# Kernel tuning notes

Measured on AMD Instinct MI355X. Metric: run time of the kernel, lower is better.

Reference implementation:

```python
import jax, jax.numpy as jnp
import numpy as np

KS = 3  # kernel_size


def _im2col(x):
    # x: (N, C, H, W) -> (N, H*W, C*KS*KS), matching torch unfold (channel-major,
    # kernel-position-minor) ordering with padding=1.
    N, C, H, W = x.shape
    xp = jnp.pad(x, ((0, 0), (0, 0), (1, 1), (1, 1)))
    patches = jnp.stack(
        [xp[:, :, i:i + H, j:j + W] for i in range(KS) for j in range(KS)],
        axis=2,
    )  # (N, C, 9, H, W)
    return patches.reshape(N, C * KS * KS, H * W).transpose(0, 2, 1)


def setup_inputs() -> dict:
    key = jax.random.key(0)
    k1, k2, k3, k4, k5 = jax.random.split(key, 5)
    N, C, H, W = 4, 64, 192, 192
    outC = 3
    return {
        "lr_features": jax.random.normal(k1, (N, C, H, W), dtype=jnp.float32),
        "W1": jax.random.normal(k2, (3, 256), dtype=jnp.float32) * 0.05,
        "b1": jax.random.normal(k3, (256,), dtype=jnp.float32) * 0.05,
        "W2": jax.random.normal(k4, (256, KS * KS * C * outC), dtype=jnp.float32) * 0.05,
        "b2": jax.random.normal(k5, (KS * KS * C * outC,), dtype=jnp.float32) * 0.05,
        "sr_scale": 4,
    }


def reference(lr_features, W1, b1, W2, b2, sr_scale):
    # Integer sr_scale: mask_mat is all-true and pos_mat_small is the s*s grid
    # of sub-pixel offsets [1/s, i/s, j/s] for i, j in [0, s).
    N, C, H, W = lr_features.shape
    s = int(np.ceil(sr_scale))
    inv = 1.0 / float(sr_scale)
    off = jnp.arange(s, dtype=jnp.float32) * inv
    pos = jnp.stack(jnp.meshgrid(off, off, indexing="ij"), axis=-1).reshape(s * s, 2)
    pos = jnp.concatenate(
        [jnp.full((s * s, 1), inv, dtype=jnp.float32), pos], axis=1
    )  # (s^2, 3)

    # Pos2Weight MLP -> per-subpixel dynamic conv weights (s^2, C*9, outC)
    hidden = jax.nn.relu(pos @ W1 + b1)
    local_weight = (hidden @ W2 + b2).reshape(s * s, KS * KS * C, -1)
    outC = local_weight.shape[-1]

    cols = _im2col(lr_features)  # (N, H*W, C*9)
    # batched small matmul: each sub-pixel position has its own filter
    out = jnp.einsum("npk,sko->nspo", cols, local_weight)  # (N, s^2, H*W, outC)
    out = out.reshape(N, s, s, H, W, outC)
    out = out.transpose(0, 5, 3, 1, 4, 2).reshape(N, outC, s * H, s * W)
    return out
```

## Files before the change

### kernel.cpp

```cpp
#include <hip/hip_runtime.h>


#define HH   192
#define WWD  192
#define SS   4
#define OC   3
#define PO   48
#define HID  256
#define W2LD 1728

typedef short  bf16x8 __attribute__((ext_vector_type(8)));
typedef float  f32x4  __attribute__((ext_vector_type(4)));

static __device__ __forceinline__ short f2bf(float f) {
    unsigned u = __float_as_uint(f);
    unsigned r = (u + 0x7fffu + ((u >> 16) & 1u)) >> 16;
    return (short)r;
}

static __device__ __forceinline__ void pin(bf16x8& v) {
    asm volatile("" : "+v"(v));
}

__global__ __launch_bounds__(256) void prep_kernel(
        const float* __restrict__ x,
        const float* __restrict__ W1, const float* __restrict__ b1,
        const float* __restrict__ W2, const float* __restrict__ b2,
        short* __restrict__ lwb, short* __restrict__ xt) {
    const int b = blockIdx.x;
    const int t = threadIdx.x;
    if (b < 112) {
        __shared__ float hlds[HID];
        const int p = b / 7;
        {
            const float pi = (float)(p >> 2) * 0.25f;
            const float pj = (float)(p & 3) * 0.25f;
            const float v = 0.25f * W1[t] + pi * W1[HID + t] + pj * W1[2 * HID + t]
                          + b1[t];
            hlds[t] = v > 0.f ? v : 0.f;
        }
        __syncthreads();
        const int col = (b % 7) * 256 + t;
        if (col < W2LD) {
            float a = 0.f;
#pragma unroll 32
            for (int hh = 0; hh < HID; ++hh)
                a += hlds[hh] * W2[hh * W2LD + col];
            const int o = col % 3, kc = col / 3;
            const int tap = kc % 9, c = kc / 9;
            lwb[(tap * PO + p * 3 + o) * 64 + c] = f2bf(a + b2[col]);
        }
    } else {
        __shared__ short tl[64][72];
        const int bb = b - 112;
        const int wt = bb % 3;
        const int h  = (bb / 3) % HH;
        const int n  = bb / (3 * HH);
        const int w0 = wt * 64;
#pragma unroll
        for (int i = 0; i < 4; ++i) {
            const int idx = i * 256 + t;
            const int c   = idx >> 4;
            const int j4  = idx & 15;
            const float4 v = *(const float4*)
                &x[(((size_t)(n * 64 + c)) * HH + h) * WWD + w0 + j4 * 4];
            tl[j4 * 4 + 0][c] = f2bf(v.x);
            tl[j4 * 4 + 1][c] = f2bf(v.y);
            tl[j4 * 4 + 2][c] = f2bf(v.z);
            tl[j4 * 4 + 3][c] = f2bf(v.w);
        }
        __syncthreads();
        const int w  = t >> 2;
        const int c0 = (t & 3) * 16;
        short* dst = &xt[(((size_t)n * HH + h) * WWD + w0 + w) * 64 + c0];
        *(bf16x8*)&dst[0] = *(const bf16x8*)&tl[w][c0];
        *(bf16x8*)&dst[8] = *(const bf16x8*)&tl[w][c0 + 8];
    }
}

__global__ __launch_bounds__(192, 3) void meta_up_mfma(
        const short* __restrict__ xt, const short* __restrict__ lwb,
        float* __restrict__ out) {
    __shared__ __align__(16) short smem[3 * 66 * 64];
    short* xlds = smem;
    float* obuf = (float*)smem;

    const int strip = (blockIdx.x & 7) * 288 + (blockIdx.x >> 3);
    const int n   = strip / (HH * 3);
    const int rem = strip % (HH * 3);
    const int h   = rem / 3;
    const int wch = rem % 3;
    const int w0  = wch * 64;

    const int tid  = threadIdx.x;
    const int lane = tid & 63, wv = tid >> 6;
    const int quad = lane >> 4, l15 = lane & 15;

    bf16x8 Bfrag[18];
#pragma unroll
    for (int tap = 0; tap < 9; ++tap)
#pragma unroll
        for (int kc2 = 0; kc2 < 2; ++kc2)
            Bfrag[tap * 2 + kc2] = *(const bf16x8*)
                &lwb[(tap * PO + wv * 16 + l15) * 64 + kc2 * 32 + quad * 8];
#pragma unroll
    for (int i = 0; i < 18; ++i) pin(Bfrag[i]);

    {
        const int gr  = h + wv - 1;
        const bool rok = (unsigned)gr < (unsigned)HH;
        const short* __restrict__ src_row =
            xt + (size_t)(n * HH + (rok ? gr : 0)) * (WWD * 64);
        const bf16x8 z = {0, 0, 0, 0, 0, 0, 0, 0};
        bf16x8 vv[8];
#pragma unroll
        for (int i = 0; i < 8; ++i) {
            const int q  = i * 64 + lane;
            const int j  = q >> 3, cb = q & 7;
            const int gc = w0 - 1 + j;
            const bool ok = rok && ((unsigned)gc < (unsigned)WWD);
            vv[i] = ok ? *(const bf16x8*)&src_row[(size_t)(ok ? gc : 0) * 64 + cb * 8]
                       : z;
        }
#pragma unroll
        for (int i = 0; i < 8; ++i) {
            const int q = i * 64 + lane;
            const int j = q >> 3, cb = q & 7;
            *(bf16x8*)&xlds[(wv * 66 + j) * 64 + ((cb ^ (j & 7)) << 3)] = vv[i];
        }
        if (lane < 16) {
            const int q  = 512 + lane;
            const int j  = q >> 3, cb = q & 7;
            const int gc = w0 - 1 + j;
            const bool ok = rok && ((unsigned)gc < (unsigned)WWD);
            const bf16x8 v = ok ?
                *(const bf16x8*)&src_row[(size_t)(ok ? gc : 0) * 64 + cb * 8] : z;
            *(bf16x8*)&xlds[(wv * 66 + j) * 64 + ((cb ^ (j & 7)) << 3)] = v;
        }
    }
    __syncthreads();

    f32x4 acc[4];
#pragma unroll
    for (int mt = 0; mt < 4; ++mt) acc[mt] = (f32x4){0.f, 0.f, 0.f, 0.f};

#pragma unroll
    for (int tap = 0; tap < 9; ++tap) {
        const int di = tap / 3, dj = tap % 3;
#pragma unroll
        for (int kc2 = 0; kc2 < 2; ++kc2) {
            const bf16x8 b = Bfrag[tap * 2 + kc2];
#pragma unroll
            for (int mt = 0; mt < 4; ++mt) {
                const int col = mt * 16 + l15 + dj;
                const int blk = (kc2 * 4 + quad) ^ (col & 7);
                bf16x8 a = *(const bf16x8*)&xlds[(di * 66 + col) * 64 + (blk << 3)];
                acc[mt] = __builtin_amdgcn_mfma_f32_16x16x32_bf16(a, b, acc[mt], 0, 0, 0);
            }
        }
    }

    __syncthreads();
    {
        const int po = wv * 16 + l15;
        const int o  = po % 3;
        const int p  = po / 3;
        const int si = p >> 2, sj = p & 3;
        const int osi = o * 4 + si;
#pragma unroll
        for (int mt = 0; mt < 4; ++mt)
#pragma unroll
            for (int r4 = 0; r4 < 4; ++r4) {
                const int wl = mt * 16 + quad * 4 + r4;
                obuf[osi * 260 + wl * 4 + sj] = acc[mt][r4];
            }
    }
    __syncthreads();
    {
        const int osi = tid >> 4;
        const int c16 = tid & 15;
        const int o = osi >> 2, si = osi & 3;
        const size_t base =
            ((size_t)(n * OC + o) * (SS * HH) + (size_t)(SS * h + si)) * (SS * WWD)
            + (size_t)(4 * w0) + c16 * 16;
        const float* __restrict__ src = &obuf[osi * 260 + c16 * 16];
#pragma unroll
        for (int i = 0; i < 4; ++i)
            *(float4*)&out[base + i * 4] = *(const float4*)&src[i * 4];
    }
}

extern "C" void kernel_launch(void* const* d_in, const int* in_sizes, int n_in,
                              void* d_out, int out_size, void* d_ws, size_t ws_size,
                              hipStream_t stream) {
    const float* x  = (const float*)d_in[0];
    const float* W1 = (const float*)d_in[1];
    const float* b1 = (const float*)d_in[2];
    const float* W2 = (const float*)d_in[3];
    const float* b2 = (const float*)d_in[4];
    float* out = (float*)d_out;
    short* lwb = (short*)d_ws;
    short* xt  = (short*)d_ws + 32768;

    prep_kernel<<<112 + 4 * HH * 3, 256, 0, stream>>>(x, W1, b1, W2, b2, lwb, xt);
    meta_up_mfma<<<4 * HH * 3, 192, 0, stream>>>(xt, lwb, out);
}
```

Baseline: 121.7 us.

## Compute three output rows per block to reuse halo rows and weight fragments

Each block of the main MFMA kernel now computes three consecutive output rows instead of one. It loads five input rows into LDS, so the vertical halo is shared and each loaded A fragment feeds up to three MFMAs. Weight fragments are now streamed through a small double buffer instead of holding all 18 in registers. The grid shrinks from 2304 to 768 blocks with more LDS per block, which cuts global and LDS traffic but leaves fewer blocks to hide latency and changes register pressure.

```diff
diff --git a/kernel.cpp b/kernel.cpp
--- a/kernel.cpp
+++ b/kernel.cpp
@@ -81,81 +81,101 @@
 __global__ __launch_bounds__(192, 3) void meta_up_mfma(
         const short* __restrict__ xt, const short* __restrict__ lwb,
         float* __restrict__ out) {
-    __shared__ __align__(16) short smem[3 * 66 * 64];
+    __shared__ __align__(16) short smem[5 * 66 * 64];
     short* xlds = smem;
     float* obuf = (float*)smem;
 
-    const int strip = (blockIdx.x & 7) * 288 + (blockIdx.x >> 3);
-    const int n   = strip / (HH * 3);
-    const int rem = strip % (HH * 3);
-    const int h   = rem / 3;
-    const int wch = rem % 3;
+    const int g   = (blockIdx.x & 7) * 96 + (blockIdx.x >> 3);
+    const int n   = g / 192;
+    const int rem = g % 192;
+    const int wch = rem / 64;
+    const int hg  = rem % 64;
+    const int h0  = hg * 3;
     const int w0  = wch * 64;
 
     const int tid  = threadIdx.x;
     const int lane = tid & 63, wv = tid >> 6;
     const int quad = lane >> 4, l15 = lane & 15;
 
-    bf16x8 Bfrag[18];
-#pragma unroll
-    for (int tap = 0; tap < 9; ++tap)
-#pragma unroll
-        for (int kc2 = 0; kc2 < 2; ++kc2)
-            Bfrag[tap * 2 + kc2] = *(const bf16x8*)
-                &lwb[(tap * PO + wv * 16 + l15) * 64 + kc2 * 32 + quad * 8];
-#pragma unroll
-    for (int i = 0; i < 18; ++i) pin(Bfrag[i]);
-
     {
-        const int gr  = h + wv - 1;
-        const bool rok = (unsigned)gr < (unsigned)HH;
-        const short* __restrict__ src_row =
-            xt + (size_t)(n * HH + (rok ? gr : 0)) * (WWD * 64);
         const bf16x8 z = {0, 0, 0, 0, 0, 0, 0, 0};
-        bf16x8 vv[8];
-#pragma unroll
-        for (int i = 0; i < 8; ++i) {
-            const int q  = i * 64 + lane;
-            const int j  = q >> 3, cb = q & 7;
-            const int gc = w0 - 1 + j;
-            const bool ok = rok && ((unsigned)gc < (unsigned)WWD);
-            vv[i] = ok ? *(const bf16x8*)&src_row[(size_t)(ok ? gc : 0) * 64 + cb * 8]
-                       : z;
-        }
-#pragma unroll
-        for (int i = 0; i < 8; ++i) {
-            const int q = i * 64 + lane;
-            const int j = q >> 3, cb = q & 7;
-            *(bf16x8*)&xlds[(wv * 66 + j) * 64 + ((cb ^ (j & 7)) << 3)] = vv[i];
-        }
-        if (lane < 16) {
-            const int q  = 512 + lane;
-            const int j  = q >> 3, cb = q & 7;
-            const int gc = w0 - 1 + j;
-            const bool ok = rok && ((unsigned)gc < (unsigned)WWD);
-            const bf16x8 v = ok ?
-                *(const bf16x8*)&src_row[(size_t)(ok ? gc : 0) * 64 + cb * 8] : z;
-            *(bf16x8*)&xlds[(wv * 66 + j) * 64 + ((cb ^ (j & 7)) << 3)] = v;
+#pragma unroll
+        for (int r0 = 0; r0 < 2; ++r0) {
+            const int r = wv + r0 * 3;
+            if (r >= 5) break;
+            const int gr  = h0 - 1 + r;
+            const bool rok = (unsigned)gr < (unsigned)HH;
+            const short* __restrict__ src_row =
+                xt + (size_t)(n * HH + (rok ? gr : 0)) * (WWD * 64);
+            bf16x8 vv[8];
+#pragma unroll
+            for (int i = 0; i < 8; ++i) {
+                const int q  = i * 64 + lane;
+                const int j  = q >> 3, cb = q & 7;
+                const int gc = w0 - 1 + j;
+                const bool ok = rok && ((unsigned)gc < (unsigned)WWD);
+                vv[i] = ok ?
+                    *(const bf16x8*)&src_row[(size_t)(ok ? gc : 0) * 64 + cb * 8] : z;
+            }
+#pragma unroll
+            for (int i = 0; i < 8; ++i) {
+                const int q = i * 64 + lane;
+                const int j = q >> 3, cb = q & 7;
+                *(bf16x8*)&xlds[(r * 66 + j) * 64 + ((cb ^ (j & 7)) << 3)] = vv[i];
+            }
+            if (lane < 16) {
+                const int q  = 512 + lane;
+                const int j  = q >> 3, cb = q & 7;
+                const int gc = w0 - 1 + j;
+                const bool ok = rok && ((unsigned)gc < (unsigned)WWD);
+                const bf16x8 v = ok ?
+                    *(const bf16x8*)&src_row[(size_t)(ok ? gc : 0) * 64 + cb * 8] : z;
+                *(bf16x8*)&xlds[(r * 66 + j) * 64 + ((cb ^ (j & 7)) << 3)] = v;
+            }
         }
     }
     __syncthreads();
 
-    f32x4 acc[4];
-#pragma unroll
-    for (int mt = 0; mt < 4; ++mt) acc[mt] = (f32x4){0.f, 0.f, 0.f, 0.f};
-
-#pragma unroll
-    for (int tap = 0; tap < 9; ++tap) {
-        const int di = tap / 3, dj = tap % 3;
-#pragma unroll
-        for (int kc2 = 0; kc2 < 2; ++kc2) {
-            const bf16x8 b = Bfrag[tap * 2 + kc2];
-#pragma unroll
-            for (int mt = 0; mt < 4; ++mt) {
-                const int col = mt * 16 + l15 + dj;
-                const int blk = (kc2 * 4 + quad) ^ (col & 7);
-                bf16x8 a = *(const bf16x8*)&xlds[(di * 66 + col) * 64 + (blk << 3)];
-                acc[mt] = __builtin_amdgcn_mfma_f32_16x16x32_bf16(a, b, acc[mt], 0, 0, 0);
+    f32x4 acc[3][4];
+#pragma unroll
+    for (int ih = 0; ih < 3; ++ih)
+#pragma unroll
+        for (int mt = 0; mt < 4; ++mt) acc[ih][mt] = (f32x4){0.f, 0.f, 0.f, 0.f};
+
+    bf16x8 Bb[2][3];
+#pragma unroll
+    for (int di = 0; di < 3; ++di) {
+        Bb[0][di] = *(const bf16x8*)
+            &lwb[((di * 3 + 0) * PO + wv * 16 + l15) * 64 + 0 * 32 + quad * 8];
+        pin(Bb[0][di]);
+    }
+
+#pragma unroll
+    for (int b = 0; b < 6; ++b) {
+        const int dj = b >> 1, kc2 = b & 1;
+        if (b < 5) {
+            const int djn = (b + 1) >> 1, kcn = (b + 1) & 1;
+#pragma unroll
+            for (int di = 0; di < 3; ++di) {
+                Bb[(b + 1) & 1][di] = *(const bf16x8*)
+                    &lwb[((di * 3 + djn) * PO + wv * 16 + l15) * 64 + kcn * 32 + quad * 8];
+                pin(Bb[(b + 1) & 1][di]);
+            }
+        }
+#pragma unroll
+        for (int mt = 0; mt < 4; ++mt) {
+            const int col = mt * 16 + l15 + dj;
+            const int blk = (kc2 * 4 + quad) ^ (col & 7);
+#pragma unroll
+            for (int r = 0; r < 5; ++r) {
+                bf16x8 a = *(const bf16x8*)&xlds[(r * 66 + col) * 64 + (blk << 3)];
+#pragma unroll
+                for (int di = 0; di < 3; ++di) {
+                    const int ih = r - di;
+                    if (ih >= 0 && ih < 3)
+                        acc[ih][mt] = __builtin_amdgcn_mfma_f32_16x16x32_bf16(
+                            a, Bb[b & 1][di], acc[ih][mt], 0, 0, 0);
+                }
             }
         }
     }
@@ -168,25 +188,31 @@
         const int si = p >> 2, sj = p & 3;
         const int osi = o * 4 + si;
 #pragma unroll
-        for (int mt = 0; mt < 4; ++mt)
-#pragma unroll
-            for (int r4 = 0; r4 < 4; ++r4) {
-                const int wl = mt * 16 + quad * 4 + r4;
-                obuf[osi * 260 + wl * 4 + sj] = acc[mt][r4];
-            }
+        for (int ih = 0; ih < 3; ++ih)
+#pragma unroll
+            for (int mt = 0; mt < 4; ++mt)
+#pragma unroll
+                for (int r4 = 0; r4 < 4; ++r4) {
+                    const int wl = mt * 16 + quad * 4 + r4;
+                    obuf[(ih * 12 + osi) * 260 + wl * 4 + sj] = acc[ih][mt][r4];
+                }
     }
     __syncthreads();
     {
         const int osi = tid >> 4;
         const int c16 = tid & 15;
         const int o = osi >> 2, si = osi & 3;
-        const size_t base =
-            ((size_t)(n * OC + o) * (SS * HH) + (size_t)(SS * h + si)) * (SS * WWD)
-            + (size_t)(4 * w0) + c16 * 16;
-        const float* __restrict__ src = &obuf[osi * 260 + c16 * 16];
-#pragma unroll
-        for (int i = 0; i < 4; ++i)
-            *(float4*)&out[base + i * 4] = *(const float4*)&src[i * 4];
+#pragma unroll
+        for (int ih = 0; ih < 3; ++ih) {
+            const int hh = h0 + ih;
+            const size_t base =
+                ((size_t)(n * OC + o) * (SS * HH) + (size_t)(SS * hh + si)) * (SS * WWD)
+                + (size_t)(4 * w0) + c16 * 16;
+            const float* __restrict__ src = &obuf[(ih * 12 + osi) * 260 + c16 * 16];
+#pragma unroll
+            for (int i = 0; i < 4; ++i)
+                *(float4*)&out[base + i * 4] = *(const float4*)&src[i * 4];
+        }
     }
 }
 
@@ -203,5 +229,5 @@
     short* xt  = (short*)d_ws + 32768;
 
     prep_kernel<<<112 + 4 * HH * 3, 256, 0, stream>>>(x, W1, b1, W2, b2, lwb, xt);
-    meta_up_mfma<<<4 * HH * 3, 192, 0, stream>>>(xt, lwb, out);
-}
+    meta_up_mfma<<<768, 192, 0, stream>>>(xt, lwb, out);
+}
```

Result: faster. 118.2 us (-2.9%).
